# Kernel optimization log

Measured on AMD Instinct MI355X. Metric: run time of the kernel, lower is better.

The kernel has to match this reference:

```python
import jax, jax.numpy as jnp
import numpy as np

U, I, D, B, E = 100000, 50000, 128, 4, 500000


def setup_inputs() -> dict:
    key = jax.random.key(0)
    ks = jax.random.split(key, 8)
    return {
        "init_user_embedding": jax.random.normal(ks[0], (U, D), dtype=jnp.float32),
        "init_item_embedding": jax.random.normal(ks[1], (I, D), dtype=jnp.float32),
        "edge_u": jax.random.randint(ks[2], (B, E), 0, U, dtype=jnp.int32),
        "edge_i": jax.random.randint(ks[3], (B, E), 0, I, dtype=jnp.int32),
        "edge_w": jax.random.uniform(ks[4], (B, E), dtype=jnp.float32),
        "u_w": jax.random.normal(ks[5], (D, D), dtype=jnp.float32) * (6.0 / (D + D)) ** 0.5,
        "i_w": jax.random.normal(ks[6], (D, D), dtype=jnp.float32) * (6.0 / (D + D)) ** 0.5,
        "alpha": jnp.full((1,), 0.25, dtype=jnp.float32),  # PReLU weight (default init 0.25)
    }


def reference(init_user_embedding, init_item_embedding, edge_u, edge_i, edge_w, u_w, i_w, alpha):
    # spmm per behavior: behavior_mats[b] @ item_emb and behavior_mats_t[b] @ user_emb
    def spmm_u(w, iu, ii):  # [U, D] = A[b] @ item_emb
        return jax.ops.segment_sum(w[:, None] * init_item_embedding[ii], iu, num_segments=U)

    def spmm_i(w, iu, ii):  # [I, D] = A[b].T @ user_emb
        return jax.ops.segment_sum(w[:, None] * init_user_embedding[iu], ii, num_segments=I)

    user_embs = jax.vmap(spmm_u)(edge_w, edge_u, edge_i)  # [B, U, D]
    item_embs = jax.vmap(spmm_i)(edge_w, edge_u, edge_i)  # [B, I, D]

    prelu = lambda x: jnp.where(x >= 0, x, alpha * x)

    multi_u = prelu(jnp.mean(user_embs, axis=0) @ u_w)    # [U, D]
    multi_i = prelu(jnp.mean(item_embs, axis=0) @ i_w)    # [I, D]
    single_u = prelu(jnp.einsum("bud,do->buo", user_embs, u_w))  # [B, U, D]
    single_i = prelu(jnp.einsum("bid,do->bio", item_embs, i_w))  # [B, I, D]
    return multi_u, multi_i, single_u, single_i
```

## Files before the change

### kernel.cpp

```cpp
#include <hip/hip_runtime.h>

#define U_N 100000
#define I_N 50000
#define D_N 128
#define B_N 4
#define E_N 500000
#define NEDGE (B_N * E_N)
#define NKEYU (4 * U_N)
#define NKEYS (NKEYU + 4 * I_N)
#define NMEMB (2 * NEDGE)
#define SCHUNK 2048
#define SNBLK ((NKEYS + SCHUNK - 1) / SCHUNK)
#define TBI ((I_N + 31) / 32)
#define TBU ((U_N + 31) / 32)
#define CB  ((NMEMB + 255) / 256)
#define NZ4 ((NKEYS + 4) / 4)
#define ZB  ((NZ4 + 255) / 256)

#define SRC_MASK 0x1FFFFu
#define W_MASK   0xFFFE0000u

typedef float f32x2 __attribute__((ext_vector_type(2)));

__device__ inline unsigned int pack_bf16(float a, float b) {
    unsigned int ua = __float_as_uint(a);
    ua += 0x7FFFu + ((ua >> 16) & 1u);
    unsigned int ub = __float_as_uint(b);
    ub += 0x7FFFu + ((ub >> 16) & 1u);
    return (ua >> 16) | (ub & 0xFFFF0000u);
}

__global__ __launch_bounds__(256) void transform2_kernel(
    const float* __restrict__ item_emb, const float* __restrict__ user_emb,
    const float* __restrict__ u_w, const float* __restrict__ i_w,
    unsigned int* __restrict__ tA, unsigned int* __restrict__ tB,
    int4* __restrict__ offs4)
{
    __shared__ float wlds[D_N][D_N];

    const float* X; const float* W; unsigned int* Y; int N; int blk;
    if (blockIdx.x < TBI) {
        X = item_emb; W = u_w; Y = tA; N = I_N; blk = blockIdx.x;
    } else if (blockIdx.x < TBI + TBU) {
        X = user_emb; W = i_w; Y = tB; N = U_N; blk = blockIdx.x - TBI;
    } else {
        int t = (blockIdx.x - TBI - TBU) * 256 + threadIdx.x;
        if (t < NZ4) offs4[t] = make_int4(0, 0, 0, 0);
        return;
    }

    for (int idx = threadIdx.x; idx < D_N * D_N / 4; idx += 256)
        reinterpret_cast<float4*>(&wlds[0][0])[idx] =
            reinterpret_cast<const float4*>(W)[idx];
    __syncthreads();

    int rr = threadIdx.x & 31;
    int cg = threadIdx.x >> 5;
    int c0 = cg * 16;
    int r  = blk * 32 + rr;
    bool valid = (r < N);
    int rc = valid ? r : (N - 1);
    const float* xrow = X + (size_t)rc * D_N;

    float4 acc[4];
    #pragma unroll
    for (int c = 0; c < 4; ++c) acc[c] = make_float4(0.f, 0.f, 0.f, 0.f);

    for (int k4 = 0; k4 < D_N / 4; ++k4) {
        float4 a = *reinterpret_cast<const float4*>(xrow + k4 * 4);
        #pragma unroll
        for (int kk = 0; kk < 4; ++kk) {
            float ak = (kk == 0) ? a.x : (kk == 1) ? a.y : (kk == 2) ? a.z : a.w;
            #pragma unroll
            for (int c = 0; c < 4; ++c) {
                const float4 wv = *reinterpret_cast<const float4*>(
                    &wlds[k4 * 4 + kk][c0 + c * 4]);
                acc[c].x += ak * wv.x;
                acc[c].y += ak * wv.y;
                acc[c].z += ak * wv.z;
                acc[c].w += ak * wv.w;
            }
        }
    }
    if (valid) {
        unsigned int* yrow = Y + (size_t)r * (D_N / 2) + c0 / 2;
        #pragma unroll
        for (int c = 0; c < 4; ++c) {
            yrow[2 * c]     = pack_bf16(acc[c].x, acc[c].y);
            yrow[2 * c + 1] = pack_bf16(acc[c].z, acc[c].w);
        }
    }
}

__global__ __launch_bounds__(256) void count_kernel(
    const int* __restrict__ eu, const int* __restrict__ ei,
    int* __restrict__ offs, int* __restrict__ rank_u, int* __restrict__ rank_i)
{
    int t = blockIdx.x * 256 + threadIdx.x;
    if (t >= NMEMB) return;
    if (t < NEDGE) {
        int e = t;
        int key = eu[e] * 4 + e / E_N;
        rank_u[e] = atomicAdd(&offs[key], 1);
    } else {
        int e = t - NEDGE;
        int key = NKEYU + ei[e] * 4 + e / E_N;
        rank_i[e] = atomicAdd(&offs[key], 1);
    }
}

__global__ __launch_bounds__(256) void scan1_kernel(
    int* __restrict__ offs, int* __restrict__ bsum)
{
    __shared__ int s[256];
    int base = blockIdx.x * SCHUNK + threadIdx.x * 8;
    int v[8]; int tsum = 0;
    #pragma unroll
    for (int j = 0; j < 8; ++j) {
        int idx = base + j;
        v[j] = (idx < NKEYS) ? offs[idx] : 0;
        tsum += v[j];
    }
    s[threadIdx.x] = tsum; __syncthreads();
    for (int off = 1; off < 256; off <<= 1) {
        int t = (threadIdx.x >= off) ? s[threadIdx.x - off] : 0;
        __syncthreads(); s[threadIdx.x] += t; __syncthreads();
    }
    int excl = s[threadIdx.x] - tsum;
    if (threadIdx.x == 255) bsum[blockIdx.x] = s[255];
    int run = excl;
    #pragma unroll
    for (int j = 0; j < 8; ++j) {
        int idx = base + j;
        if (idx < NKEYS) offs[idx] = run;
        run += v[j];
    }
}

__global__ __launch_bounds__(512) void scan2_kernel(int* __restrict__ bsum,
                                                    int* __restrict__ offs)
{
    __shared__ int s[512];
    int v = (threadIdx.x < SNBLK) ? bsum[threadIdx.x] : 0;
    s[threadIdx.x] = v; __syncthreads();
    for (int off = 1; off < 512; off <<= 1) {
        int t = (threadIdx.x >= off) ? s[threadIdx.x - off] : 0;
        __syncthreads(); s[threadIdx.x] += t; __syncthreads();
    }
    if (threadIdx.x < SNBLK) bsum[threadIdx.x] = s[threadIdx.x] - v;
    if (threadIdx.x == 511) offs[NKEYS] = s[511];
}

__global__ __launch_bounds__(256) void scan3_kernel(int* __restrict__ offs,
                                                    const int* __restrict__ bsum)
{
    int add = bsum[blockIdx.x];
    int base = blockIdx.x * SCHUNK + threadIdx.x * 8;
    #pragma unroll
    for (int j = 0; j < 8; ++j) {
        int idx = base + j;
        if (idx < NKEYS) offs[idx] += add;
    }
}

__global__ __launch_bounds__(256) void fill_kernel(
    const int* __restrict__ eu, const int* __restrict__ ei,
    const float* __restrict__ ew,
    const int* __restrict__ offs,
    const int* __restrict__ rank_u, const int* __restrict__ rank_i,
    unsigned int* __restrict__ pairs)
{
    int t = blockIdx.x * 256 + threadIdx.x;
    if (t >= NMEMB) return;
    if (t < NEDGE) {
        int e = t;
        int b = e / E_N;
        int key = eu[e] * 4 + b;
        int pos = offs[key] + rank_u[e];
        unsigned int wb = __float_as_uint(ew[e]) + 0x10000u;
        pairs[pos] = (wb & W_MASK) | (unsigned int)ei[e];
    } else {
        int e = t - NEDGE;
        int b = e / E_N;
        int key = NKEYU + ei[e] * 4 + b;
        int pos = offs[key] + rank_i[e];
        unsigned int wb = __float_as_uint(ew[e]) + 0x10000u;
        pairs[pos] = (wb & W_MASK) | (unsigned int)eu[e];
    }
}

__global__ __launch_bounds__(256) void gather_kernel(
    const unsigned int* __restrict__ T,
    const unsigned int* __restrict__ pairs, const int* __restrict__ offs,
    float* __restrict__ single, float* __restrict__ multi,
    int N, int keybase, const float* __restrict__ alpha_p)
{
    int r = blockIdx.x * 4 + (threadIdx.x >> 6);
    if (r >= N) return;
    int k0 = keybase + r * 4;

    float alpha = alpha_p[0];
    int lane = threadIdx.x & 63;

    int o0 = __builtin_amdgcn_readfirstlane(offs[k0]);
    int o1 = __builtin_amdgcn_readfirstlane(offs[k0 + 1]);
    int o2 = __builtin_amdgcn_readfirstlane(offs[k0 + 2]);
    int o3 = __builtin_amdgcn_readfirstlane(offs[k0 + 3]);
    int o4 = __builtin_amdgcn_readfirstlane(offs[k0 + 4]);
    int p0 = o0, p1 = o1, p2 = o2, p3 = o3;

    float ax0 = 0.f, ay0 = 0.f, ax1 = 0.f, ay1 = 0.f;
    float ax2 = 0.f, ay2 = 0.f, ax3 = 0.f, ay3 = 0.f;

    while ((p0 < o1) | (p1 < o2) | (p2 < o3) | (p3 < o4)) {
        int a0 = p0 < o1, b0 = (p0 + 1) < o1;
        int a1 = p1 < o2, b1 = (p1 + 1) < o2;
        int a2 = p2 < o3, b2 = (p2 + 1) < o3;
        int a3 = p3 < o4, b3 = (p3 + 1) < o4;
        int i0a = a0 ? p0 : o0;         int i0b = b0 ? (p0 + 1) : i0a;
        int i1a = a1 ? p1 : o0;         int i1b = b1 ? (p1 + 1) : i1a;
        int i2a = a2 ? p2 : o0;         int i2b = b2 ? (p2 + 1) : i2a;
        int i3a = a3 ? p3 : o0;         int i3b = b3 ? (p3 + 1) : i3a;
        unsigned int s0a = __builtin_amdgcn_readfirstlane(pairs[i0a]);
        unsigned int s0b = __builtin_amdgcn_readfirstlane(pairs[i0b]);
        unsigned int s1a = __builtin_amdgcn_readfirstlane(pairs[i1a]);
        unsigned int s1b = __builtin_amdgcn_readfirstlane(pairs[i1b]);
        unsigned int s2a = __builtin_amdgcn_readfirstlane(pairs[i2a]);
        unsigned int s2b = __builtin_amdgcn_readfirstlane(pairs[i2b]);
        unsigned int s3a = __builtin_amdgcn_readfirstlane(pairs[i3a]);
        unsigned int s3b = __builtin_amdgcn_readfirstlane(pairs[i3b]);
        unsigned int d0a = T[(size_t)(s0a & SRC_MASK) * (D_N / 2) + lane];
        unsigned int d0b = T[(size_t)(s0b & SRC_MASK) * (D_N / 2) + lane];
        unsigned int d1a = T[(size_t)(s1a & SRC_MASK) * (D_N / 2) + lane];
        unsigned int d1b = T[(size_t)(s1b & SRC_MASK) * (D_N / 2) + lane];
        unsigned int d2a = T[(size_t)(s2a & SRC_MASK) * (D_N / 2) + lane];
        unsigned int d2b = T[(size_t)(s2b & SRC_MASK) * (D_N / 2) + lane];
        unsigned int d3a = T[(size_t)(s3a & SRC_MASK) * (D_N / 2) + lane];
        unsigned int d3b = T[(size_t)(s3b & SRC_MASK) * (D_N / 2) + lane];
        float w0a = a0 ? __uint_as_float(s0a & W_MASK) : 0.f;
        float w0b = b0 ? __uint_as_float(s0b & W_MASK) : 0.f;
        float w1a = a1 ? __uint_as_float(s1a & W_MASK) : 0.f;
        float w1b = b1 ? __uint_as_float(s1b & W_MASK) : 0.f;
        float w2a = a2 ? __uint_as_float(s2a & W_MASK) : 0.f;
        float w2b = b2 ? __uint_as_float(s2b & W_MASK) : 0.f;
        float w3a = a3 ? __uint_as_float(s3a & W_MASK) : 0.f;
        float w3b = b3 ? __uint_as_float(s3b & W_MASK) : 0.f;
        ax0 += w0a * __uint_as_float(d0a << 16)
             + w0b * __uint_as_float(d0b << 16);
        ay0 += w0a * __uint_as_float(d0a & 0xFFFF0000u)
             + w0b * __uint_as_float(d0b & 0xFFFF0000u);
        ax1 += w1a * __uint_as_float(d1a << 16)
             + w1b * __uint_as_float(d1b << 16);
        ay1 += w1a * __uint_as_float(d1a & 0xFFFF0000u)
             + w1b * __uint_as_float(d1b & 0xFFFF0000u);
        ax2 += w2a * __uint_as_float(d2a << 16)
             + w2b * __uint_as_float(d2b << 16);
        ay2 += w2a * __uint_as_float(d2a & 0xFFFF0000u)
             + w2b * __uint_as_float(d2b & 0xFFFF0000u);
        ax3 += w3a * __uint_as_float(d3a << 16)
             + w3b * __uint_as_float(d3b << 16);
        ay3 += w3a * __uint_as_float(d3a & 0xFFFF0000u)
             + w3b * __uint_as_float(d3b & 0xFFFF0000u);
        p0 += a0 + b0; p1 += a1 + b1; p2 += a2 + b2; p3 += a3 + b3;
    }

    float mx = 0.25f * (ax0 + ax1 + ax2 + ax3);
    float my = 0.25f * (ay0 + ay1 + ay2 + ay3);

    f32x2 o;
    o.x = ax0 >= 0.f ? ax0 : alpha * ax0;
    o.y = ay0 >= 0.f ? ay0 : alpha * ay0;
    __builtin_nontemporal_store(o, reinterpret_cast<f32x2*>(
        single + ((size_t)0 * N + r) * D_N + lane * 2));
    o.x = ax1 >= 0.f ? ax1 : alpha * ax1;
    o.y = ay1 >= 0.f ? ay1 : alpha * ay1;
    __builtin_nontemporal_store(o, reinterpret_cast<f32x2*>(
        single + ((size_t)1 * N + r) * D_N + lane * 2));
    o.x = ax2 >= 0.f ? ax2 : alpha * ax2;
    o.y = ay2 >= 0.f ? ay2 : alpha * ay2;
    __builtin_nontemporal_store(o, reinterpret_cast<f32x2*>(
        single + ((size_t)2 * N + r) * D_N + lane * 2));
    o.x = ax3 >= 0.f ? ax3 : alpha * ax3;
    o.y = ay3 >= 0.f ? ay3 : alpha * ay3;
    __builtin_nontemporal_store(o, reinterpret_cast<f32x2*>(
        single + ((size_t)3 * N + r) * D_N + lane * 2));

    o.x = mx >= 0.f ? mx : alpha * mx;
    o.y = my >= 0.f ? my : alpha * my;
    __builtin_nontemporal_store(o, reinterpret_cast<f32x2*>(
        multi + (size_t)r * D_N + lane * 2));
}

extern "C" void kernel_launch(void* const* d_in, const int* in_sizes, int n_in,
                              void* d_out, int out_size, void* d_ws, size_t ws_size,
                              hipStream_t stream) {
    const float* user_emb = (const float*)d_in[0];
    const float* item_emb = (const float*)d_in[1];
    const int*   eu       = (const int*)d_in[2];
    const int*   ei       = (const int*)d_in[3];
    const float* ew       = (const float*)d_in[4];
    const float* u_w      = (const float*)d_in[5];
    const float* i_w      = (const float*)d_in[6];
    const float* alpha    = (const float*)d_in[7];

    float* out      = (float*)d_out;
    float* multi_u  = out;
    float* multi_i  = out + (size_t)U_N * D_N;
    float* single_u = out + (size_t)(U_N + I_N) * D_N;
    float* single_i = single_u + (size_t)B_N * U_N * D_N;

    int* rank_u = (int*)multi_i;
    int* rank_i = rank_u + NEDGE;

    int*  offs  = (int*)d_ws;
    int*  bsum  = offs + (NKEYS + 4);
    unsigned int* pairs =
        (unsigned int*)((char*)d_ws + ((((NKEYS + 4 + 512) * 4) + 255) & ~255));
    unsigned int* tA = pairs + NMEMB;
    unsigned int* tB = tA + (size_t)I_N * (D_N / 2);

    transform2_kernel<<<TBI + TBU + ZB, 256, 0, stream>>>(
        item_emb, user_emb, u_w, i_w, tA, tB, (int4*)offs);
    count_kernel<<<CB, 256, 0, stream>>>(eu, ei, offs, rank_u, rank_i);
    scan1_kernel<<<SNBLK, 256, 0, stream>>>(offs, bsum);
    scan2_kernel<<<1, 512, 0, stream>>>(bsum, offs);
    scan3_kernel<<<SNBLK, 256, 0, stream>>>(offs, bsum);
    fill_kernel<<<CB, 256, 0, stream>>>(eu, ei, ew, offs,
                                        rank_u, rank_i, pairs);
    gather_kernel<<<(U_N + 3) / 4, 256, 0, stream>>>(
        tA, pairs, offs, single_u, multi_u, U_N, 0, alpha);
    gather_kernel<<<(I_N + 3) / 4, 256, 0, stream>>>(
        tB, pairs, offs, single_i, multi_i, I_N, NKEYU, alpha);
}
```

Baseline: 545.5 us.

## Use bf16 MFMA for the dense embedding-by-weight transform

Measured after the change: 445.5 us. 18.3% less time.

```diff
diff --git a/kernel.cpp b/kernel.cpp
--- a/kernel.cpp
+++ b/kernel.cpp
@@ -11,16 +11,20 @@
 #define NMEMB (2 * NEDGE)
 #define SCHUNK 2048
 #define SNBLK ((NKEYS + SCHUNK - 1) / SCHUNK)
-#define TBI ((I_N + 31) / 32)
-#define TBU ((U_N + 31) / 32)
 #define CB  ((NMEMB + 255) / 256)
 #define NZ4 ((NKEYS + 4) / 4)
 #define ZB  ((NZ4 + 255) / 256)
+#define TB2I ((I_N + 63) / 64)
+#define TB2U ((U_N + 63) / 64)
 
 #define SRC_MASK 0x1FFFFu
 #define W_MASK   0xFFFE0000u
 
 typedef float f32x2 __attribute__((ext_vector_type(2)));
+typedef float f32x4 __attribute__((ext_vector_type(4)));
+typedef short bf16x8 __attribute__((ext_vector_type(8)));
+typedef unsigned int u32x4 __attribute__((ext_vector_type(4)));
+typedef unsigned int u32x2 __attribute__((ext_vector_type(2)));
 
 __device__ inline unsigned int pack_bf16(float a, float b) {
     unsigned int ua = __float_as_uint(a);
@@ -30,65 +34,79 @@
     return (ua >> 16) | (ub & 0xFFFF0000u);
 }
 
-__global__ __launch_bounds__(256) void transform2_kernel(
+__global__ __launch_bounds__(256) void transform_mfma_kernel(
     const float* __restrict__ item_emb, const float* __restrict__ user_emb,
     const float* __restrict__ u_w, const float* __restrict__ i_w,
     unsigned int* __restrict__ tA, unsigned int* __restrict__ tB,
     int4* __restrict__ offs4)
 {
-    __shared__ float wlds[D_N][D_N];
+    __shared__ short wf[2048 * 8];
 
     const float* X; const float* W; unsigned int* Y; int N; int blk;
-    if (blockIdx.x < TBI) {
+    if (blockIdx.x < TB2I) {
         X = item_emb; W = u_w; Y = tA; N = I_N; blk = blockIdx.x;
-    } else if (blockIdx.x < TBI + TBU) {
-        X = user_emb; W = i_w; Y = tB; N = U_N; blk = blockIdx.x - TBI;
+    } else if (blockIdx.x < TB2I + TB2U) {
+        X = user_emb; W = i_w; Y = tB; N = U_N; blk = blockIdx.x - TB2I;
     } else {
-        int t = (blockIdx.x - TBI - TBU) * 256 + threadIdx.x;
+        int t = (blockIdx.x - TB2I - TB2U) * 256 + threadIdx.x;
         if (t < NZ4) offs4[t] = make_int4(0, 0, 0, 0);
         return;
     }
 
-    for (int idx = threadIdx.x; idx < D_N * D_N / 4; idx += 256)
-        reinterpret_cast<float4*>(&wlds[0][0])[idx] =
-            reinterpret_cast<const float4*>(W)[idx];
+    for (int f = threadIdx.x; f < 2048; f += 256) {
+        int kt = f >> 9;
+        int l  = f & 63;
+        int c  = ((f >> 6) & 7) * 16 + (l & 15);
+        int kb = kt * 32 + ((l >> 4) << 3);
+        u32x4 q;
+        q.x = pack_bf16(W[(kb + 0) * D_N + c], W[(kb + 1) * D_N + c]);
+        q.y = pack_bf16(W[(kb + 2) * D_N + c], W[(kb + 3) * D_N + c]);
+        q.z = pack_bf16(W[(kb + 4) * D_N + c], W[(kb + 5) * D_N + c]);
+        q.w = pack_bf16(W[(kb + 6) * D_N + c], W[(kb + 7) * D_N + c]);
+        *reinterpret_cast<u32x4*>(&wf[f * 8]) = q;
+    }
     __syncthreads();
 
-    int rr = threadIdx.x & 31;
-    int cg = threadIdx.x >> 5;
-    int c0 = cg * 16;
-    int r  = blk * 32 + rr;
-    bool valid = (r < N);
-    int rc = valid ? r : (N - 1);
-    const float* xrow = X + (size_t)rc * D_N;
-
-    float4 acc[4];
-    #pragma unroll
-    for (int c = 0; c < 4; ++c) acc[c] = make_float4(0.f, 0.f, 0.f, 0.f);
-
-    for (int k4 = 0; k4 < D_N / 4; ++k4) {
-        float4 a = *reinterpret_cast<const float4*>(xrow + k4 * 4);
+    int wave = threadIdx.x >> 6;
+    int lane = threadIdx.x & 63;
+    int rowbase = blk * 64 + wave * 16;
+    if (rowbase >= N) return;
+
+    f32x4 acc[8];
+    #pragma unroll
+    for (int ct = 0; ct < 8; ++ct) acc[ct] = (f32x4){0.f, 0.f, 0.f, 0.f};
+
+    const float* xr0 = X + (size_t)(rowbase + (lane & 15)) * D_N
+                         + ((lane >> 4) << 3);
+    #pragma unroll
+    for (int kt = 0; kt < 4; ++kt) {
+        const float* xr = xr0 + kt * 32;
+        float4 x0 = *reinterpret_cast<const float4*>(xr);
+        float4 x1 = *reinterpret_cast<const float4*>(xr + 4);
+        u32x4 bu;
+        bu.x = pack_bf16(x0.x, x0.y);
+        bu.y = pack_bf16(x0.z, x0.w);
+        bu.z = pack_bf16(x1.x, x1.y);
+        bu.w = pack_bf16(x1.z, x1.w);
+        bf16x8 bfrag = __builtin_bit_cast(bf16x8, bu);
         #pragma unroll
-        for (int kk = 0; kk < 4; ++kk) {
-            float ak = (kk == 0) ? a.x : (kk == 1) ? a.y : (kk == 2) ? a.z : a.w;
-            #pragma unroll
-            for (int c = 0; c < 4; ++c) {
-                const float4 wv = *reinterpret_cast<const float4*>(
-                    &wlds[k4 * 4 + kk][c0 + c * 4]);
-                acc[c].x += ak * wv.x;
-                acc[c].y += ak * wv.y;
-                acc[c].z += ak * wv.z;
-                acc[c].w += ak * wv.w;
-            }
+        for (int ct = 0; ct < 8; ++ct) {
+            bf16x8 afrag = *reinterpret_cast<const bf16x8*>(
+                &wf[(((kt * 8 + ct) * 64) + lane) * 8]);
+            acc[ct] = __builtin_amdgcn_mfma_f32_16x16x32_bf16(
+                afrag, bfrag, acc[ct], 0, 0, 0);
         }
     }
-    if (valid) {
-        unsigned int* yrow = Y + (size_t)r * (D_N / 2) + c0 / 2;
-        #pragma unroll
-        for (int c = 0; c < 4; ++c) {
-            yrow[2 * c]     = pack_bf16(acc[c].x, acc[c].y);
-            yrow[2 * c + 1] = pack_bf16(acc[c].z, acc[c].w);
-        }
+
+    int row = rowbase + (lane & 15);
+    int qd  = lane >> 4;
+    unsigned int* yrow = Y + (size_t)row * (D_N / 2);
+    #pragma unroll
+    for (int ct = 0; ct < 8; ++ct) {
+        u32x2 yy;
+        yy.x = pack_bf16(acc[ct][0], acc[ct][1]);
+        yy.y = pack_bf16(acc[ct][2], acc[ct][3]);
+        *reinterpret_cast<u32x2*>(yrow + ct * 8 + qd * 2) = yy;
     }
 }
 
@@ -319,7 +337,7 @@
     unsigned int* tA = pairs + NMEMB;
     unsigned int* tB = tA + (size_t)I_N * (D_N / 2);
 
-    transform2_kernel<<<TBI + TBU + ZB, 256, 0, stream>>>(
+    transform_mfma_kernel<<<TB2I + TB2U + ZB, 256, 0, stream>>>(
         item_emb, user_emb, u_w, i_w, tA, tB, (int4*)offs);
     count_kernel<<<CB, 256, 0, stream>>>(eu, ei, offs, rank_u, rank_i);
     scan1_kernel<<<SNBLK, 256, 0, stream>>>(offs, bsum);
```
